# Kernel optimization log

Hardware: AMD Instinct MI355X
Metric: run time of the kernel (lower is better)

The kernel has to match this reference:

```python
import jax, jax.numpy as jnp
import numpy as np

ALPHA = 1e-4
MARGIN = 100.0
K = 3
DROP_P = 0.7


def setup_inputs() -> dict:
    key = jax.random.key(0)
    ks = jax.random.split(key, 8)
    NC, B, T, F = 10, 32, 200, 2048
    return {
        "abnr_feat_magn": jax.random.uniform(ks[0], (B, T), jnp.float32),
        "norm_feat_magn": jax.random.uniform(ks[1], (B, T), jnp.float32),
        "abnr_feats": jax.random.normal(ks[2], (NC, B, T, F), jnp.float32),
        "norm_feats": jax.random.normal(ks[3], (NC, B, T, F), jnp.float32),
        "abnr_sls": jax.random.uniform(ks[4], (B, T), jnp.float32),
        "norm_sls": jax.random.uniform(ks[5], (B, T), jnp.float32),
        "abnr_drop_u": jax.random.uniform(ks[6], (B, T), jnp.float32),
        "norm_drop_u": jax.random.uniform(ks[7], (B, T), jnp.float32),
    }


def _topk_idx(magn, drop_u):
    # Dropout(0.7) on ones_like, multiplied into the magnitudes before top-k.
    mask = (drop_u >= DROP_P).astype(magn.dtype) / (1.0 - DROP_P)
    _, idx = jax.lax.top_k(magn * mask, K)  # (B, K)
    return idx


def _gather_mean_norm(feats, idx):
    # feats: (NC, B, T, F); idx: (B, K) -> gather over T per crop, mean over K, L2 over F.
    sel = jnp.take_along_axis(feats, idx[None, :, :, None], axis=2)  # (NC, B, K, F)
    mean_feat = sel.mean(axis=2)  # (NC, B, F)  == torch.cat over crops -> (NC*B, F)
    return jnp.linalg.norm(mean_feat, axis=-1).reshape(-1)  # (NC*B,)


def _clamped_log(x):
    # torch BCELoss clamps log terms at -100
    return jnp.clip(jnp.log(x), -100.0, None)


def reference(abnr_feat_magn, norm_feat_magn, abnr_feats, norm_feats,
              abnr_sls, norm_sls, abnr_drop_u, norm_drop_u):
    idx_abnr = _topk_idx(abnr_feat_magn, abnr_drop_u)  # (B, K)
    idx_norm = _topk_idx(norm_feat_magn, norm_drop_u)

    l2_abn = _gather_mean_norm(abnr_feats, idx_abnr)   # (NC*B,)
    l2_nor = _gather_mean_norm(norm_feats, idx_norm)
    loss_abn = jnp.abs(MARGIN - l2_abn)
    loss_rtfm = jnp.mean((loss_abn + l2_nor) ** 2)

    vls_abn = jnp.take_along_axis(abnr_sls, idx_abnr, axis=1).mean(axis=1)  # (B,)
    vls_nor = jnp.take_along_axis(norm_sls, idx_norm, axis=1).mean(axis=1)
    loss_bcea = -jnp.mean(_clamped_log(vls_abn))          # BCE vs target 1
    loss_bcen = -jnp.mean(_clamped_log(1.0 - vls_nor))    # BCE vs target 0
    loss_vls = loss_bcea + loss_bcen

    return ALPHA * loss_rtfm, loss_vls
```

## Files before the change

### kernel.cpp

```cpp
#include <hip/hip_runtime.h>
#include <math.h>

#define BB 32
#define TT 200
#define NCC 10
#define FF 2048
#define KK 3
#define NBLK (2 * NCC * BB * 2)

__device__ inline void wave_argmax(float& v, int& i) {
    #pragma unroll
    for (int m = 1; m < 64; m <<= 1) {
        float ov = __shfl_xor(v, m);
        int   oi = __shfl_xor(i, m);
        if (ov > v || (ov == v && oi < i)) { v = ov; i = oi; }
    }
}

__device__ inline float wave_sum(float v) {
    #pragma unroll
    for (int m = 1; m < 64; m <<= 1) v += __shfl_xor(v, m);
    return v;
}

__global__ __launch_bounds__(256) void fused_kernel(
        const float* __restrict__ abnr_magn,
        const float* __restrict__ norm_magn,
        const float* __restrict__ abnr_feats,
        const float* __restrict__ norm_feats,
        const float* __restrict__ abnr_sls,
        const float* __restrict__ norm_sls,
        const float* __restrict__ abnr_u,
        const float* __restrict__ norm_u,
        float* __restrict__ partial ,
        float* __restrict__ bce     ) {
    const int blk  = blockIdx.x;
    const int fc   = blk & 1;
    const int r    = blk >> 1;
    const int b    = r % BB;
    const int sn   = r / BB;
    const int side = sn / NCC;
    const int nc   = sn % NCC;
    const int tid  = threadIdx.x;
    const int lane = tid & 63;
    const int wav  = tid >> 6;

    const float* feats = side ? norm_feats : abnr_feats;

    __shared__ int   s_idx[KK];
    __shared__ float s_red[4];

    int id0, id1, id2;

    if (wav == 0) {
        const float* magn = side ? norm_magn : abnr_magn;
        const float* u    = side ? norm_u    : abnr_u;
        const float scale = 1.0f / (1.0f - 0.7f);
        float vv[4];
        int   tv[4];
        #pragma unroll
        for (int j = 0; j < 4; ++j) {
            int t = lane + 64 * j;
            if (t < TT) {
                float m = (u[b * TT + t] >= 0.7f) ? scale : 0.0f;
                vv[j] = magn[b * TT + t] * m;
                tv[j] = t;
            } else {
                vv[j] = -INFINITY;
                tv[j] = 1 << 30;
            }
        }
        int id[KK];
        #pragma unroll
        for (int k = 0; k < KK; ++k) {
            float bv = -INFINITY;
            int   bi = 1 << 30;
            #pragma unroll
            for (int j = 0; j < 4; ++j)
                if (vv[j] > bv || (vv[j] == bv && tv[j] < bi)) { bv = vv[j]; bi = tv[j]; }
            wave_argmax(bv, bi);
            id[k] = bi;
            #pragma unroll
            for (int j = 0; j < 4; ++j)
                if (tv[j] == bi) vv[j] = -INFINITY;
        }
        if (lane < KK) s_idx[lane] = id[lane];

        if (nc == 0 && fc == 0 && lane == 0) {
            const float* sls = side ? norm_sls : abnr_sls;
            float v = (sls[b * TT + id[0]] + sls[b * TT + id[1]] +
                       sls[b * TT + id[2]]) * (1.0f / 3.0f);
            bce[side * BB + b] = side ? fmaxf(logf(1.0f - v), -100.0f)
                                      : fmaxf(logf(v), -100.0f);
        }
    }
    __syncthreads();
    id0 = s_idx[0]; id1 = s_idx[1]; id2 = s_idx[2];

    const size_t base = (size_t)(nc * BB + b) * (TT * FF) + (size_t)fc * (FF / 2) + tid * 4;
    float4 x0 = *(const float4*)(feats + base + (size_t)id0 * FF);
    float4 x1 = *(const float4*)(feats + base + (size_t)id1 * FF);
    float4 x2 = *(const float4*)(feats + base + (size_t)id2 * FF);
    float m0 = x0.x + x1.x + x2.x;
    float m1 = x0.y + x1.y + x2.y;
    float m2 = x0.z + x1.z + x2.z;
    float m3 = x0.w + x1.w + x2.w;
    float acc = m0 * m0 + m1 * m1 + m2 * m2 + m3 * m3;

    acc = wave_sum(acc);
    if (lane == 0) s_red[wav] = acc;
    __syncthreads();
    if (tid == 0)
        partial[blk] = s_red[0] + s_red[1] + s_red[2] + s_red[3];
}

__global__ __launch_bounds__(256) void final_kernel(
        const float* __restrict__ partial, const float* __restrict__ bce,
        float* __restrict__ out) {
    __shared__ float sA[4], sB[4];
    const int tid  = threadIdx.x;
    const int lane = tid & 63;
    const int wav  = tid >> 6;
    const float third = 1.0f / 3.0f;

    float s = 0.0f;
    for (int i = tid; i < NCC * BB; i += 256) {
        float pa = partial[2 * i] + partial[2 * i + 1];
        float pn = partial[2 * (NCC * BB + i)] + partial[2 * (NCC * BB + i) + 1];
        float l2a = sqrtf(pa) * third;
        float l2n = sqrtf(pn) * third;
        float t = fabsf(100.0f - l2a) + l2n;
        s += t * t;
    }
    s = wave_sum(s);
    if (lane == 0) sA[wav] = s;

    float s2 = (tid < 2 * BB) ? bce[tid] : 0.0f;
    s2 = wave_sum(s2);
    if (lane == 0) sB[wav] = s2;
    __syncthreads();

    if (tid == 0) {
        float loss_rtfm = (sA[0] + sA[1] + sA[2] + sA[3]) * (1.0f / (float)(NCC * BB));
        float bsum = sB[0] + sB[1] + sB[2] + sB[3];
        out[0] = 1e-4f * loss_rtfm;
        out[1] = -bsum * (1.0f / (float)BB);
    }
}

extern "C" void kernel_launch(void* const* d_in, const int* in_sizes, int n_in,
                              void* d_out, int out_size, void* d_ws, size_t ws_size,
                              hipStream_t stream) {
    const float* abnr_magn  = (const float*)d_in[0];
    const float* norm_magn  = (const float*)d_in[1];
    const float* abnr_feats = (const float*)d_in[2];
    const float* norm_feats = (const float*)d_in[3];
    const float* abnr_sls   = (const float*)d_in[4];
    const float* norm_sls   = (const float*)d_in[5];
    const float* abnr_u     = (const float*)d_in[6];
    const float* norm_u     = (const float*)d_in[7];
    float* out = (float*)d_out;

    float* bce     = (float*)d_ws;
    float* partial = (float*)((char*)d_ws + 4096);

    fused_kernel<<<NBLK, 256, 0, stream>>>(abnr_magn, norm_magn,
                                           abnr_feats, norm_feats,
                                           abnr_sls, norm_sls,
                                           abnr_u, norm_u,
                                           partial, bce);
    final_kernel<<<1, 256, 0, stream>>>(partial, bce, out);
}
```

Measured before the change: 11.89 us.

## Use single-wave blocks so every wave does its own top-k, dropping LDS syncs

The fused kernel now launches 64-thread blocks (one wavefront), and twice as many of them, with each block covering a quarter of the feature row using two float4 loads per lane per index. Every wave computes the top-k itself from float4-vectorized magnitude and dropout loads, which removes the shared-memory index broadcast and both __syncthreads. The final kernel likewise becomes a single wave reading four partials per row as a float4. The cost is doing the top-k work redundantly in four times as many blocks, in exchange for removing the serialization where three waves idled while one did the top-k.

```diff
diff --git a/kernel.cpp b/kernel.cpp
--- a/kernel.cpp
+++ b/kernel.cpp
@@ -6,7 +6,7 @@
 #define NCC 10
 #define FF 2048
 #define KK 3
-#define NBLK (2 * NCC * BB * 2)
+#define NBLK (2 * NCC * BB * 4)
 
 __device__ inline void wave_argmax(float& v, int& i) {
     #pragma unroll
@@ -23,7 +23,7 @@
     return v;
 }
 
-__global__ __launch_bounds__(256) void fused_kernel(
+__global__ __launch_bounds__(64) void fused_kernel(
         const float* __restrict__ abnr_magn,
         const float* __restrict__ norm_magn,
         const float* __restrict__ abnr_feats,
@@ -35,116 +35,109 @@
         float* __restrict__ partial ,
         float* __restrict__ bce     ) {
     const int blk  = blockIdx.x;
-    const int fc   = blk & 1;
-    const int r    = blk >> 1;
+    const int fc   = blk & 3;
+    const int r    = blk >> 2;
     const int b    = r % BB;
     const int sn   = r / BB;
     const int side = sn / NCC;
     const int nc   = sn % NCC;
-    const int tid  = threadIdx.x;
-    const int lane = tid & 63;
-    const int wav  = tid >> 6;
+    const int lane = threadIdx.x;
 
     const float* feats = side ? norm_feats : abnr_feats;
+    const float* magn  = side ? norm_magn  : abnr_magn;
+    const float* u     = side ? norm_u     : abnr_u;
 
-    __shared__ int   s_idx[KK];
-    __shared__ float s_red[4];
+    const float scale = 1.0f / (1.0f - 0.7f);
+    float vv[4];
+    int   tv[4];
+    if (lane < TT / 4) {
+        float4 mg = *(const float4*)(magn + b * TT + lane * 4);
+        float4 uu = *(const float4*)(u    + b * TT + lane * 4);
+        vv[0] = mg.x * ((uu.x >= 0.7f) ? scale : 0.0f);
+        vv[1] = mg.y * ((uu.y >= 0.7f) ? scale : 0.0f);
+        vv[2] = mg.z * ((uu.z >= 0.7f) ? scale : 0.0f);
+        vv[3] = mg.w * ((uu.w >= 0.7f) ? scale : 0.0f);
+        #pragma unroll
+        for (int j = 0; j < 4; ++j) tv[j] = lane * 4 + j;
+    } else {
+        #pragma unroll
+        for (int j = 0; j < 4; ++j) { vv[j] = -INFINITY; tv[j] = 1 << 30; }
+    }
+    int id[KK];
+    #pragma unroll
+    for (int k = 0; k < KK; ++k) {
+        float bv = -INFINITY;
+        int   bi = 1 << 30;
+        #pragma unroll
+        for (int j = 0; j < 4; ++j)
+            if (vv[j] > bv || (vv[j] == bv && tv[j] < bi)) { bv = vv[j]; bi = tv[j]; }
+        wave_argmax(bv, bi);
+        id[k] = bi;
+        #pragma unroll
+        for (int j = 0; j < 4; ++j)
+            if (tv[j] == bi) vv[j] = -INFINITY;
+    }
 
-    int id0, id1, id2;
+    const size_t base = (size_t)(nc * BB + b) * (TT * FF) + (size_t)fc * (FF / 4) + lane * 4;
+    const float* p0 = feats + base + (size_t)id[0] * FF;
+    const float* p1 = feats + base + (size_t)id[1] * FF;
+    const float* p2 = feats + base + (size_t)id[2] * FF;
+    float4 a0 = *(const float4*)(p0);
+    float4 a1 = *(const float4*)(p1);
+    float4 a2 = *(const float4*)(p2);
+    float4 b0 = *(const float4*)(p0 + 256);
+    float4 b1 = *(const float4*)(p1 + 256);
+    float4 b2 = *(const float4*)(p2 + 256);
 
-    if (wav == 0) {
-        const float* magn = side ? norm_magn : abnr_magn;
-        const float* u    = side ? norm_u    : abnr_u;
-        const float scale = 1.0f / (1.0f - 0.7f);
-        float vv[4];
-        int   tv[4];
-        #pragma unroll
-        for (int j = 0; j < 4; ++j) {
-            int t = lane + 64 * j;
-            if (t < TT) {
-                float m = (u[b * TT + t] >= 0.7f) ? scale : 0.0f;
-                vv[j] = magn[b * TT + t] * m;
-                tv[j] = t;
-            } else {
-                vv[j] = -INFINITY;
-                tv[j] = 1 << 30;
-            }
-        }
-        int id[KK];
-        #pragma unroll
-        for (int k = 0; k < KK; ++k) {
-            float bv = -INFINITY;
-            int   bi = 1 << 30;
-            #pragma unroll
-            for (int j = 0; j < 4; ++j)
-                if (vv[j] > bv || (vv[j] == bv && tv[j] < bi)) { bv = vv[j]; bi = tv[j]; }
-            wave_argmax(bv, bi);
-            id[k] = bi;
-            #pragma unroll
-            for (int j = 0; j < 4; ++j)
-                if (tv[j] == bi) vv[j] = -INFINITY;
-        }
-        if (lane < KK) s_idx[lane] = id[lane];
-
-        if (nc == 0 && fc == 0 && lane == 0) {
-            const float* sls = side ? norm_sls : abnr_sls;
-            float v = (sls[b * TT + id[0]] + sls[b * TT + id[1]] +
-                       sls[b * TT + id[2]]) * (1.0f / 3.0f);
-            bce[side * BB + b] = side ? fmaxf(logf(1.0f - v), -100.0f)
-                                      : fmaxf(logf(v), -100.0f);
-        }
-    }
-    __syncthreads();
-    id0 = s_idx[0]; id1 = s_idx[1]; id2 = s_idx[2];
-
-    const size_t base = (size_t)(nc * BB + b) * (TT * FF) + (size_t)fc * (FF / 2) + tid * 4;
-    float4 x0 = *(const float4*)(feats + base + (size_t)id0 * FF);
-    float4 x1 = *(const float4*)(feats + base + (size_t)id1 * FF);
-    float4 x2 = *(const float4*)(feats + base + (size_t)id2 * FF);
-    float m0 = x0.x + x1.x + x2.x;
-    float m1 = x0.y + x1.y + x2.y;
-    float m2 = x0.z + x1.z + x2.z;
-    float m3 = x0.w + x1.w + x2.w;
-    float acc = m0 * m0 + m1 * m1 + m2 * m2 + m3 * m3;
+    float m, acc = 0.0f;
+    m = a0.x + a1.x + a2.x; acc += m * m;
+    m = a0.y + a1.y + a2.y; acc += m * m;
+    m = a0.z + a1.z + a2.z; acc += m * m;
+    m = a0.w + a1.w + a2.w; acc += m * m;
+    m = b0.x + b1.x + b2.x; acc += m * m;
+    m = b0.y + b1.y + b2.y; acc += m * m;
+    m = b0.z + b1.z + b2.z; acc += m * m;
+    m = b0.w + b1.w + b2.w; acc += m * m;
 
     acc = wave_sum(acc);
-    if (lane == 0) s_red[wav] = acc;
-    __syncthreads();
-    if (tid == 0)
-        partial[blk] = s_red[0] + s_red[1] + s_red[2] + s_red[3];
+    if (lane == 0) partial[blk] = acc;
+
+    if (nc == 0 && fc == 0 && lane == 0) {
+        const float* sls = side ? norm_sls : abnr_sls;
+        float v = (sls[b * TT + id[0]] + sls[b * TT + id[1]] +
+                   sls[b * TT + id[2]]) * (1.0f / 3.0f);
+        bce[side * BB + b] = side ? fmaxf(logf(1.0f - v), -100.0f)
+                                  : fmaxf(logf(v), -100.0f);
+    }
 }
 
-__global__ __launch_bounds__(256) void final_kernel(
+__global__ __launch_bounds__(64) void final_kernel(
         const float* __restrict__ partial, const float* __restrict__ bce,
         float* __restrict__ out) {
-    __shared__ float sA[4], sB[4];
-    const int tid  = threadIdx.x;
-    const int lane = tid & 63;
-    const int wav  = tid >> 6;
+    const int lane = threadIdx.x;
     const float third = 1.0f / 3.0f;
 
     float s = 0.0f;
-    for (int i = tid; i < NCC * BB; i += 256) {
-        float pa = partial[2 * i] + partial[2 * i + 1];
-        float pn = partial[2 * (NCC * BB + i)] + partial[2 * (NCC * BB + i) + 1];
+    #pragma unroll
+    for (int it = 0; it < (NCC * BB) / 64; ++it) {
+        int i = it * 64 + lane;
+        float4 pa4 = *(const float4*)(partial + 4 * i);
+        float4 pn4 = *(const float4*)(partial + 4 * (NCC * BB + i));
+        float pa = (pa4.x + pa4.y) + (pa4.z + pa4.w);
+        float pn = (pn4.x + pn4.y) + (pn4.z + pn4.w);
         float l2a = sqrtf(pa) * third;
         float l2n = sqrtf(pn) * third;
         float t = fabsf(100.0f - l2a) + l2n;
         s += t * t;
     }
     s = wave_sum(s);
-    if (lane == 0) sA[wav] = s;
 
-    float s2 = (tid < 2 * BB) ? bce[tid] : 0.0f;
+    float s2 = bce[lane];
     s2 = wave_sum(s2);
-    if (lane == 0) sB[wav] = s2;
-    __syncthreads();
 
-    if (tid == 0) {
-        float loss_rtfm = (sA[0] + sA[1] + sA[2] + sA[3]) * (1.0f / (float)(NCC * BB));
-        float bsum = sB[0] + sB[1] + sB[2] + sB[3];
-        out[0] = 1e-4f * loss_rtfm;
-        out[1] = -bsum * (1.0f / (float)BB);
+    if (lane == 0) {
+        out[0] = 1e-4f * (s * (1.0f / (float)(NCC * BB)));
+        out[1] = -s2 * (1.0f / (float)BB);
     }
 }
 
@@ -164,10 +157,10 @@
     float* bce     = (float*)d_ws;
     float* partial = (float*)((char*)d_ws + 4096);
 
-    fused_kernel<<<NBLK, 256, 0, stream>>>(abnr_magn, norm_magn,
-                                           abnr_feats, norm_feats,
-                                           abnr_sls, norm_sls,
-                                           abnr_u, norm_u,
-                                           partial, bce);
-    final_kernel<<<1, 256, 0, stream>>>(partial, bce, out);
+    fused_kernel<<<NBLK, 64, 0, stream>>>(abnr_magn, norm_magn,
+                                          abnr_feats, norm_feats,
+                                          abnr_sls, norm_sls,
+                                          abnr_u, norm_u,
+                                          partial, bce);
+    final_kernel<<<1, 64, 0, stream>>>(partial, bce, out);
 }
```

Result: no change. 12.03 us (+1.1%).
